# Performance work log

Measured on AMD Instinct MI355X. Metric: run time of the kernel, lower is better.

Reference implementation:

```python
import jax, jax.numpy as jnp
import numpy as np

B, S, DIM = 1, 4096, 4096
H, HL, D = 32, 8, 128          # query heads, kv heads (GQA), head_dim
BS = 8                          # sparse_block_size
SINK_TOK, WIN_TOK = 30, 30
HEAVY = 800                     # heavy_const -> Mb = HEAVY // BS top blocks
NEG = -1e30


def setup_inputs() -> dict:
    key = jax.random.key(0)
    k0, k1, k2, k3 = jax.random.split(key, 4)
    x = jax.random.normal(k0, (B, S, DIM), jnp.float32)
    freqs_cis = jax.random.uniform(k1, (S, D // 2, 2), jnp.float32)  # (cos,sin)-like pairs
    wqkv_w = jax.random.normal(k2, ((H + 2 * HL) * D, DIM), jnp.float32) * 0.02
    wo_w = jax.random.normal(k3, (DIM, DIM), jnp.float32) * 0.02
    input_pos = jnp.arange(S, dtype=jnp.int32)
    return {"x": x, "freqs_cis": freqs_cis, "wqkv_w": wqkv_w, "wo_w": wo_w, "input_pos": input_pos}


def _rope(x, fc):
    # x: [B,S,h,D], fc: [S,D/2,2]
    xr = x.reshape(*x.shape[:-1], -1, 2)            # [B,S,h,D/2,2]
    fc = fc[None, :, None]                           # [1,S,1,D/2,2]
    out = jnp.stack([xr[..., 0] * fc[..., 0] - xr[..., 1] * fc[..., 1],
                     xr[..., 1] * fc[..., 0] + xr[..., 0] * fc[..., 1]], axis=-1)
    return out.reshape(x.shape)


def reference(x, freqs_cis, wqkv_w, wo_w, input_pos):
    rep = H // HL
    Tb = (S + BS - 1) // BS
    scale = 1.0 / jnp.sqrt(jnp.float32(D))

    qkv = x @ wqkv_w.T                               # [B,S,(H+2HL)*D]
    q, k, v = jnp.split(qkv, [H * D, (H + HL) * D], axis=-1)
    q = q.reshape(B, S, H, D)
    k = k.reshape(B, S, HL, D)
    v = v.reshape(B, S, HL, D)
    q = _rope(q, freqs_cis)
    k = _rope(k, freqs_cis)

    # ---- block accumulators (KVCache.update_tokens), vectorized ----
    blk = input_pos // BS                            # [S]
    k_sum = jax.ops.segment_sum(jnp.swapaxes(k, 0, 1), blk, num_segments=Tb)  # [Tb,B,HL,D]
    cnt = jax.ops.segment_sum(jnp.ones((S,), jnp.float32), blk, num_segments=Tb)  # [Tb]
    k_rep = k_sum / jnp.maximum(cnt, 1.0)[:, None, None, None]                # block-mean keys
    k_rep_h = jnp.repeat(k_rep, rep, axis=2)        # [Tb,B,H,D] (GQA repeat)

    # ---- per-(B,H) block routing scores ----
    q_mean = q.mean(axis=1)                          # [B,H,D]
    scores = jnp.einsum('bhd,tbhd->bht', q_mean, k_rep_h) * scale  # [B,H,Tb]
    scores = jnp.where(cnt[None, None, :] > 0, scores, NEG)

    # ---- build_block_index: sink + window + topk ----
    sink_b = min((min(SINK_TOK, S) + BS - 1) // BS, Tb)
    window_b = min((min(WIN_TOK, S) + BS - 1) // BS, Tb)
    cur_block = (S - 1) // BS
    win_start = max(0, cur_block - window_b + 1)
    win_end = cur_block + 1
    sink_ids = jnp.arange(sink_b, dtype=jnp.int32)
    window_ids = jnp.arange(win_start, win_end, dtype=jnp.int32)
    Mb = max(0, min(HEAVY // BS, Tb))
    sc = scores.at[..., :sink_b].set(NEG).at[..., window_ids].set(NEG)
    top_ids = jax.lax.top_k(sc, Mb)[1].astype(jnp.int32)                      # [B,H,Mb]
    bidx = jnp.concatenate([
        jnp.broadcast_to(sink_ids, (B, H, sink_b)),
        jnp.broadcast_to(window_ids, (B, H, win_end - win_start)),
        top_ids], axis=-1)                           # [B,H,KLIST]

    # ---- gather selected block tokens ----
    tok = bidx[..., None] * BS + jnp.arange(BS, dtype=jnp.int32)              # [B,H,KLIST,BS]
    KL = bidx.shape[-1]
    tok = tok.reshape(B, H, KL * BS)                 # [B,H,Kt]
    valid = (tok >= 0) & (tok < S)
    tok_c = jnp.clip(tok, 0, S - 1)

    k_bhsd = jnp.swapaxes(jnp.repeat(k, rep, axis=2), 1, 2)  # [B,H,S,D]
    v_bhsd = jnp.swapaxes(jnp.repeat(v, rep, axis=2), 1, 2)
    Ksel = jnp.take_along_axis(k_bhsd, tok_c[..., None], axis=2)  # [B,H,Kt,D]
    Vsel = jnp.take_along_axis(v_bhsd, tok_c[..., None], axis=2)

    # ---- block-sparse attention with causal mask ----
    q_bhsd = jnp.swapaxes(q, 1, 2)                   # [B,H,S,D]
    att = jnp.einsum('bhsd,bhkd->bhsk', q_bhsd, Ksel) * scale
    mask = (tok_c[:, :, None, :] <= input_pos[None, None, :, None]) & valid[:, :, None, :]
    att = jnp.where(mask, att, NEG)
    p = jax.nn.softmax(att, axis=-1)
    out = jnp.einsum('bhsk,bhkd->bhsd', p, Vsel)     # [B,H,S,D]
    y = jnp.swapaxes(out, 1, 2).reshape(B, S, H * D) @ wo_w.T
    return y
```

## Files before the change

### kernel.cpp

```cpp
#include <hip/hip_runtime.h>
#include <hip/hip_bf16.h>

typedef unsigned short u16;
typedef unsigned int   u32;

using bf16x8 = __attribute__((ext_vector_type(8))) short;
using f32x4  = __attribute__((ext_vector_type(4))) float;

constexpr int S = 4096, DIM = 4096, H = 32, HL = 8, D = 128;
constexpr int NQKV = (H + 2 * HL) * D;
constexpr int QVW = (H + HL) * D;
constexpr int TB = S / 8;
constexpr int KL = 108;
constexpr float NEGF = -1e30f;
constexpr float SCALE = 0.08838834764831845f;

__device__ inline float bflo(u32 u) { return __builtin_bit_cast(float, u << 16); }
__device__ inline float bfhi(u32 u) { return __builtin_bit_cast(float, u & 0xFFFF0000u); }
__device__ inline u16 rne16(float f) {
  u32 b = __builtin_bit_cast(u32, f);
  return (u16)((b + 0x7FFFu + ((b >> 16) & 1u)) >> 16);
}
__device__ inline float bf2f(u16 h) { return __builtin_bit_cast(float, (u32)h << 16); }
__device__ inline u32 pk2(u16 a, u16 b) { return (u32)a | ((u32)b << 16); }

__device__ __forceinline__ void gload16(const u16* g, u16* l) {
  __builtin_amdgcn_global_load_lds(
      (__attribute__((address_space(1))) void*)g,
      (__attribute__((address_space(3))) void*)l, 16, 0, 0);
}

__device__ inline void xcd_swz(int nx, int& bx, int& by) {
  const int flat = blockIdx.y * nx + blockIdx.x;
  const int nwg = nx * gridDim.y;
  const int cpx = nwg >> 3;
  const int s = (flat & 7) * cpx + (flat >> 3);
  bx = s % nx;
  by = s / nx;
}

__global__ __launch_bounds__(256) void split_f32_kernel(
    const float* __restrict__ src, u16* __restrict__ hi, u16* __restrict__ lo) {
  const size_t i = ((size_t)blockIdx.x * 256 + threadIdx.x) * 8;
  float4 v0 = *(const float4*)(src + i);
  float4 v1 = *(const float4*)(src + i + 4);
  float f[8] = {v0.x, v0.y, v0.z, v0.w, v1.x, v1.y, v1.z, v1.w};
  u16 h[8], l[8];
#pragma unroll
  for (int j = 0; j < 8; ++j) {
    h[j] = rne16(f[j]);
    l[j] = rne16(f[j] - bf2f(h[j]));
  }
  uint4 ph, pl;
  ph.x = pk2(h[0], h[1]); ph.y = pk2(h[2], h[3]);
  ph.z = pk2(h[4], h[5]); ph.w = pk2(h[6], h[7]);
  pl.x = pk2(l[0], l[1]); pl.y = pk2(l[2], l[3]);
  pl.z = pk2(l[4], l[5]); pl.w = pk2(l[6], l[7]);
  *(uint4*)(hi + i) = ph;
  *(uint4*)(lo + i) = pl;
}

__global__ __launch_bounds__(256) void conv_wqkv_kernel(
    const float* __restrict__ src, u16* __restrict__ wqv,
    u16* __restrict__ wkh, u16* __restrict__ wkl) {
  const size_t i = ((size_t)blockIdx.x * 256 + threadIdx.x) * 8;
  float4 v0 = *(const float4*)(src + i);
  float4 v1 = *(const float4*)(src + i + 4);
  float f[8] = {v0.x, v0.y, v0.z, v0.w, v1.x, v1.y, v1.z, v1.w};
  u16 h[8];
#pragma unroll
  for (int j = 0; j < 8; ++j) h[j] = rne16(f[j]);
  uint4 ph;
  ph.x = pk2(h[0], h[1]); ph.y = pk2(h[2], h[3]);
  ph.z = pk2(h[4], h[5]); ph.w = pk2(h[6], h[7]);
  const int row = (int)(i >> 12);
  if (row < H * D) {
    *(uint4*)(wqv + i) = ph;
  } else if (row < (H + HL) * D) {
    const size_t off = i - (size_t)(H * D) * DIM;
    u16 l[8];
#pragma unroll
    for (int j = 0; j < 8; ++j) l[j] = rne16(f[j] - bf2f(h[j]));
    uint4 pl;
    pl.x = pk2(l[0], l[1]); pl.y = pk2(l[2], l[3]);
    pl.z = pk2(l[4], l[5]); pl.w = pk2(l[6], l[7]);
    *(uint4*)(wkh + off) = ph;
    *(uint4*)(wkl + off) = pl;
  } else {
    *(uint4*)(wqv + (i - (size_t)(HL * D) * DIM)) = ph;
  }
}

__global__ __launch_bounds__(256) void cast_bf16_kernel(
    const float* __restrict__ src, u16* __restrict__ dst) {
  const size_t i = ((size_t)blockIdx.x * 256 + threadIdx.x) * 8;
  float4 v0 = *(const float4*)(src + i);
  float4 v1 = *(const float4*)(src + i + 4);
  uint4 ph;
  ph.x = pk2(rne16(v0.x), rne16(v0.y));
  ph.y = pk2(rne16(v0.z), rne16(v0.w));
  ph.z = pk2(rne16(v1.x), rne16(v1.y));
  ph.w = pk2(rne16(v1.z), rne16(v1.w));
  *(uint4*)(dst + i) = ph;
}

template <bool OBF16>
__global__ __launch_bounds__(512, 2) void gemm256(
    const u16* __restrict__ A, const u16* __restrict__ B,
    void* __restrict__ Cp, int M, int N, int K, int lda, int ldb, int ldc) {
  __shared__ u16 lds[4 * 16384];
  const int tid = threadIdx.x;
  const int w = tid >> 6, lane = tid & 63;
  const int wm = w >> 2, wn = w & 3;
  const int l15 = lane & 15, g = lane >> 4;
  int bx, by;
  xcd_swz(gridDim.x, bx, by);
  const int m0 = by * 256, n0 = bx * 256;

  const u16* ga[4];
  const u16* gb[4];
#pragma unroll
  for (int r = 0; r < 4; ++r) {
    const int c = r * 512 + tid;
    const int row = c >> 3, j = c & 7;
    const int jsw = j ^ (row & 7);
    ga[r] = A + (size_t)(m0 + row) * lda + jsw * 8;
    gb[r] = B + (size_t)(n0 + row) * ldb + jsw * 8;
  }

  auto stageA = [&](int buf, int kt) {
    u16* base = lds + buf * 32768 + w * 512;
#pragma unroll
    for (int r = 0; r < 4; ++r) gload16(ga[r] + kt * 64, base + r * 4096);
  };
  auto stageB = [&](int buf, int kt) {
    u16* base = lds + buf * 32768 + 16384 + w * 512;
#pragma unroll
    for (int r = 0; r < 4; ++r) gload16(gb[r] + kt * 64, base + r * 4096);
  };

  bf16x8 afr[4][2], bfr[2][2];
  auto loadA = [&](int buf, int q) {
    const u16* Ab = lds + buf * 32768;
#pragma unroll
    for (int fr = 0; fr < 4; ++fr) {
      const int row = wm * 128 + q * 64 + fr * 16 + l15;
#pragma unroll
      for (int kh = 0; kh < 2; ++kh)
        afr[fr][kh] = *(const bf16x8*)(Ab + row * 64 + ((((kh << 2) | g)) ^ (l15 & 7)) * 8);
    }
  };
  auto loadB = [&](int buf, int r2) {
    const u16* Bb = lds + buf * 32768 + 16384;
#pragma unroll
    for (int fc = 0; fc < 2; ++fc) {
      const int row = wn * 64 + r2 * 32 + fc * 16 + l15;
#pragma unroll
      for (int kh = 0; kh < 2; ++kh)
        bfr[fc][kh] = *(const bf16x8*)(Bb + row * 64 + ((((kh << 2) | g)) ^ (l15 & 7)) * 8);
    }
  };

  f32x4 acc[8][4];
#pragma unroll
  for (int i = 0; i < 8; ++i)
#pragma unroll
    for (int j = 0; j < 4; ++j) acc[i][j] = {0.f, 0.f, 0.f, 0.f};

  auto mma = [&](int q, int r2) {
    __builtin_amdgcn_s_setprio(1);
#pragma unroll
    for (int fr = 0; fr < 4; ++fr)
#pragma unroll
      for (int fc = 0; fc < 2; ++fc)
#pragma unroll
        for (int kh = 0; kh < 2; ++kh)
          acc[q * 4 + fr][r2 * 2 + fc] = __builtin_amdgcn_mfma_f32_16x16x32_bf16(
              afr[fr][kh], bfr[fc][kh], acc[q * 4 + fr][r2 * 2 + fc], 0, 0, 0);
    __builtin_amdgcn_s_setprio(0);
  };

  stageA(0, 0);
  stageB(0, 0);
  const int NT = K / 64;
  for (int t = 0; t < NT; ++t) {
    const int cur = t & 1, nxt = cur ^ 1;
    if (t + 1 < NT) {
      stageA(nxt, t + 1);
      asm volatile("s_waitcnt vmcnt(4)" ::: "memory");
    } else {
      asm volatile("s_waitcnt vmcnt(0)" ::: "memory");
    }
    __builtin_amdgcn_sched_barrier(0);
    __builtin_amdgcn_s_barrier();
    loadA(cur, 0);
    loadB(cur, 0);
    mma(0, 0);
    __builtin_amdgcn_s_barrier();
    loadA(cur, 1);
    if (t + 1 < NT) stageB(nxt, t + 1);
    __builtin_amdgcn_s_barrier();
    mma(1, 0);
    __builtin_amdgcn_s_barrier();
    loadA(cur, 0);
    loadB(cur, 1);
    __builtin_amdgcn_s_barrier();
    mma(0, 1);
    __builtin_amdgcn_s_barrier();
    loadA(cur, 1);
    __builtin_amdgcn_s_barrier();
    mma(1, 1);
    __builtin_amdgcn_s_barrier();
  }
#pragma unroll
  for (int mf = 0; mf < 8; ++mf)
#pragma unroll
    for (int nf = 0; nf < 4; ++nf)
#pragma unroll
      for (int rg = 0; rg < 4; ++rg) {
        const int row = m0 + wm * 128 + mf * 16 + g * 4 + rg;
        const int col = n0 + wn * 64 + nf * 16 + l15;
        if constexpr (OBF16)
          ((u16*)Cp)[(size_t)row * ldc + col] = rne16(acc[mf][nf][rg]);
        else
          ((float*)Cp)[(size_t)row * ldc + col] = acc[mf][nf][rg];
      }
}

template <bool OBF16>
__global__ __launch_bounds__(256) void gemm_bf16(
    const u16* __restrict__ A, const u16* __restrict__ B,
    void* __restrict__ Cp, int M, int N, int K, int lda, int ldb, int ldc) {
  __shared__ u16 As[2][128 * 32];
  __shared__ u16 Bs[2][128 * 32];
  const int tid = threadIdx.x;
  const int lane = tid & 63;
  const int w = tid >> 6;
  const int wm = w >> 1, wn = w & 1;
  int bx, by;
  xcd_swz(gridDim.x, bx, by);
  const int m0 = by * 128, n0 = bx * 128;
  const int l15 = lane & 15, g = lane >> 4;
  const int srow = tid >> 2;
  const int scol = (tid & 3) * 8;

  const u16* ga = A + (size_t)(m0 + srow) * lda + scol;
  const u16* gb = B + (size_t)(n0 + srow) * ldb + scol;
  const size_t a64 = (size_t)64 * lda;
  const size_t b64 = (size_t)64 * ldb;

  auto stage = [&](int buf, int k0) {
    u16* lA = As[buf] + w * 512;
    u16* lB = Bs[buf] + w * 512;
    gload16(ga + k0, lA);
    gload16(ga + k0 + a64, lA + 2048);
    gload16(gb + k0, lB);
    gload16(gb + k0 + b64, lB + 2048);
  };

  f32x4 acc[4][4];
#pragma unroll
  for (int i = 0; i < 4; ++i)
#pragma unroll
    for (int j = 0; j < 4; ++j) acc[i][j] = {0.f, 0.f, 0.f, 0.f};

  stage(0, 0);
  __syncthreads();
  const int niter = K / 32;
  for (int it = 0; it < niter; ++it) {
    const int cur = it & 1;
    if (it + 1 < niter) stage(cur ^ 1, (it + 1) * 32);
    bf16x8 af[4], bfr[4];
#pragma unroll
    for (int i = 0; i < 4; ++i)
      af[i] = *(const bf16x8*)(As[cur] + (wm * 64 + i * 16 + l15) * 32 + g * 8);
#pragma unroll
    for (int j = 0; j < 4; ++j)
      bfr[j] = *(const bf16x8*)(Bs[cur] + (wn * 64 + j * 16 + l15) * 32 + g * 8);
#pragma unroll
    for (int i = 0; i < 4; ++i)
#pragma unroll
      for (int j = 0; j < 4; ++j)
        acc[i][j] = __builtin_amdgcn_mfma_f32_16x16x32_bf16(af[i], bfr[j], acc[i][j], 0, 0, 0);
    __syncthreads();
  }
#pragma unroll
  for (int i = 0; i < 4; ++i)
#pragma unroll
    for (int j = 0; j < 4; ++j)
#pragma unroll
      for (int rg = 0; rg < 4; ++rg) {
        const int row = m0 + wm * 64 + i * 16 + g * 4 + rg;
        const int col = n0 + wn * 64 + j * 16 + l15;
        if constexpr (OBF16)
          ((u16*)Cp)[(size_t)row * ldc + col] = rne16(acc[i][j][rg]);
        else
          ((float*)Cp)[(size_t)row * ldc + col] = acc[i][j][rg];
      }
}

__global__ __launch_bounds__(256) void gemm_k3(
    const u16* __restrict__ Ahg, const u16* __restrict__ Alg,
    const u16* __restrict__ Bhg, const u16* __restrict__ Blg,
    float* __restrict__ C, int M, int N, int K) {
  __shared__ u16 Ah[2][128 * 32];
  __shared__ u16 Al[2][128 * 32];
  __shared__ u16 Bh[2][64 * 32];
  __shared__ u16 Bl[2][64 * 32];
  const int tid = threadIdx.x;
  const int lane = tid & 63;
  const int w = tid >> 6;
  const int wm = w >> 1, wn = w & 1;
  int bx, by;
  xcd_swz(gridDim.x, bx, by);
  const int m0 = by * 128, n0 = bx * 64;
  const int l15 = lane & 15, g = lane >> 4;
  const int srow = tid >> 2;
  const int scol = (tid & 3) * 8;

  const u16* gah = Ahg + (size_t)(m0 + srow) * K + scol;
  const u16* gal = Alg + (size_t)(m0 + srow) * K + scol;
  const u16* gbh = Bhg + (size_t)(n0 + srow) * K + scol;
  const u16* gbl = Blg + (size_t)(n0 + srow) * K + scol;
  const size_t a64 = (size_t)64 * K;

  auto stage = [&](int buf, int k0) {
    gload16(gah + k0, Ah[buf] + w * 512);
    gload16(gah + k0 + a64, Ah[buf] + w * 512 + 2048);
    gload16(gal + k0, Al[buf] + w * 512);
    gload16(gal + k0 + a64, Al[buf] + w * 512 + 2048);
    gload16(gbh + k0, Bh[buf] + w * 512);
    gload16(gbl + k0, Bl[buf] + w * 512);
  };

  f32x4 acc[4][2];
#pragma unroll
  for (int i = 0; i < 4; ++i)
#pragma unroll
    for (int j = 0; j < 2; ++j) acc[i][j] = {0.f, 0.f, 0.f, 0.f};

  stage(0, 0);
  __syncthreads();
  const int niter = K / 32;
  for (int it = 0; it < niter; ++it) {
    const int cur = it & 1;
    if (it + 1 < niter) stage(cur ^ 1, (it + 1) * 32);
    bf16x8 fah[4], fal[4], fbh[2], fbl[2];
#pragma unroll
    for (int i = 0; i < 4; ++i) {
      fah[i] = *(const bf16x8*)(Ah[cur] + (wm * 64 + i * 16 + l15) * 32 + g * 8);
      fal[i] = *(const bf16x8*)(Al[cur] + (wm * 64 + i * 16 + l15) * 32 + g * 8);
    }
#pragma unroll
    for (int j = 0; j < 2; ++j) {
      fbh[j] = *(const bf16x8*)(Bh[cur] + (wn * 32 + j * 16 + l15) * 32 + g * 8);
      fbl[j] = *(const bf16x8*)(Bl[cur] + (wn * 32 + j * 16 + l15) * 32 + g * 8);
    }
#pragma unroll
    for (int i = 0; i < 4; ++i)
#pragma unroll
      for (int j = 0; j < 2; ++j) {
        acc[i][j] = __builtin_amdgcn_mfma_f32_16x16x32_bf16(fal[i], fbh[j], acc[i][j], 0, 0, 0);
        acc[i][j] = __builtin_amdgcn_mfma_f32_16x16x32_bf16(fah[i], fbl[j], acc[i][j], 0, 0, 0);
        acc[i][j] = __builtin_amdgcn_mfma_f32_16x16x32_bf16(fah[i], fbh[j], acc[i][j], 0, 0, 0);
      }
    __syncthreads();
  }
#pragma unroll
  for (int i = 0; i < 4; ++i)
#pragma unroll
    for (int j = 0; j < 2; ++j)
#pragma unroll
      for (int rg = 0; rg < 4; ++rg) {
        const int row = m0 + wm * 64 + i * 16 + g * 4 + rg;
        const int col = n0 + wn * 32 + j * 16 + l15;
        C[(size_t)row * N + col] = acc[i][j][rg];
      }
}

__global__ __launch_bounds__(128) void xcd_kernel(
    const float* __restrict__ x, const float* __restrict__ freqs,
    float* __restrict__ XC, float* __restrict__ XD) {
  const int d = blockIdx.x * 128 + threadIdx.x;
  const int i0 = blockIdx.y * 32;
  const int s0 = blockIdx.z * 128;
  float accC[32], accD[32];
#pragma unroll
  for (int ii = 0; ii < 32; ++ii) { accC[ii] = 0.f; accD[ii] = 0.f; }
  for (int s = s0; s < s0 + 128; ++s) {
    const float xv = x[(size_t)s * DIM + d];
    const float* fr = freqs + (size_t)s * 128 + i0 * 2;
#pragma unroll
    for (int ii = 0; ii < 32; ++ii) {
      accC[ii] += fr[2 * ii] * xv;
      accD[ii] += fr[2 * ii + 1] * xv;
    }
  }
#pragma unroll
  for (int ii = 0; ii < 32; ++ii) {
    atomicAdd(&XC[(size_t)(i0 + ii) * DIM + d], accC[ii]);
    atomicAdd(&XD[(size_t)(i0 + ii) * DIM + d], accD[ii]);
  }
}

__global__ __launch_bounds__(256) void mrow_kernel(
    const float* __restrict__ wq, const float* __restrict__ XC,
    const float* __restrict__ XD, float* __restrict__ M1, float* __restrict__ M2) {
  const int r = blockIdx.x * 4 + (threadIdx.x >> 6);
  const int lane = threadIdx.x & 63;
  const int i = (r & 127) >> 1;
  const float* wr = wq + (size_t)r * DIM;
  const float* xc = XC + (size_t)i * DIM;
  const float* xd = XD + (size_t)i * DIM;
  float s1 = 0.f, s2 = 0.f;
  for (int k = lane; k < DIM; k += 64) {
    float wv = wr[k];
    s1 += wv * xc[k];
    s2 += wv * xd[k];
  }
#pragma unroll
  for (int off = 1; off < 64; off <<= 1) {
    s1 += __shfl_xor(s1, off, 64);
    s2 += __shfl_xor(s2, off, 64);
  }
  if (lane == 0) { M1[r] = s1; M2[r] = s2; }
}

__global__ __launch_bounds__(256) void rope_q_kernel(
    const u16* __restrict__ qvb, const float* __restrict__ freqs,
    u16* __restrict__ qb) {
  const int h = blockIdx.y;
  const int s0 = blockIdx.x * 64;
  const int tid = threadIdx.x;
  const int d = tid & 127, half = tid >> 7;
  for (int pp = half; pp < 64; pp += 2) {
    const int s = s0 + pp;
    u32 pr = *(const u32*)(qvb + (size_t)s * QVW + h * D + (d & ~1));
    float a = bflo(pr), b = bfhi(pr);
    float2 fc = *(const float2*)(freqs + (size_t)s * 128 + (d & ~1));
    float o = (d & 1) ? (b * fc.x + a * fc.y) : (a * fc.x - b * fc.y);
    qb[((size_t)h * S + s) * D + d] = rne16(o);
  }
}

__global__ __launch_bounds__(128) void rope_kv_kernel(
    const float* __restrict__ kf, const u16* __restrict__ qvb,
    const float* __restrict__ freqs,
    u16* __restrict__ kb, u16* __restrict__ vbt, float* __restrict__ krep) {
  const int hl = blockIdx.y;
  const int t = blockIdx.x;
  const int d = threadIdx.x;
  float sum = 0.f;
  u16 vv[8];
#pragma unroll
  for (int pp = 0; pp < 8; ++pp) {
    const int s = t * 8 + pp;
    float2 kp = *(const float2*)(kf + (size_t)s * 1024 + hl * D + (d & ~1));
    float2 fc = *(const float2*)(freqs + (size_t)s * 128 + (d & ~1));
    float o = (d & 1) ? (kp.y * fc.x + kp.x * fc.y) : (kp.x * fc.x - kp.y * fc.y);
    kb[((size_t)hl * S + s) * D + d] = rne16(o);
    sum += o;
    vv[pp] = qvb[(size_t)s * QVW + H * D + hl * D + d];
  }
  krep[((size_t)t * HL + hl) * D + d] = sum * 0.125f;
  uint4 pk;
  pk.x = pk2(vv[0], vv[1]);
  pk.y = pk2(vv[2], vv[3]);
  pk.z = pk2(vv[4], vv[5]);
  pk.w = pk2(vv[6], vv[7]);
  *(uint4*)(vbt + ((size_t)hl * D + d) * S + t * 8) = pk;
}

__global__ __launch_bounds__(512) void topk_kernel(
    const float* __restrict__ M1, const float* __restrict__ M2,
    const float* __restrict__ krep, int* __restrict__ bidx) {
  const int h = blockIdx.x;
  const int t = threadIdx.x;
  __shared__ float qm[128];
  if (t < 128) {
    int r = h * 128 + t;
    float v = (t & 1) ? (M1[r] + M2[r - 1]) : (M1[r] - M2[r + 1]);
    qm[t] = v * (1.f / 4096.f);
  }
  __syncthreads();
  const float* kr = krep + ((size_t)t * HL + (h >> 2)) * 128;
  float s = 0.f;
#pragma unroll 8
  for (int d = 0; d < 128; ++d) s += qm[d] * kr[d];
  s *= SCALE;
  if (t < 4 || t >= 508) s = NEGF;
  if (t < 4) {
    bidx[h * KL + t] = t;
    bidx[h * KL + 4 + t] = 508 + t;
  }
  __shared__ float wv[8];
  __shared__ int wi[8];
  __shared__ int bestsh;
  for (int iter = 0; iter < 100; ++iter) {
    float v = s;
    int idx = t;
#pragma unroll
    for (int off = 1; off < 64; off <<= 1) {
      float ov = __shfl_xor(v, off, 64);
      int oi = __shfl_xor(idx, off, 64);
      if (ov > v || (ov == v && oi < idx)) { v = ov; idx = oi; }
    }
    if ((t & 63) == 0) { wv[t >> 6] = v; wi[t >> 6] = idx; }
    __syncthreads();
    if (t == 0) {
      float bv = wv[0];
      int bi = wi[0];
#pragma unroll
      for (int u = 1; u < 8; ++u)
        if (wv[u] > bv || (wv[u] == bv && wi[u] < bi)) { bv = wv[u]; bi = wi[u]; }
      bestsh = bi;
      bidx[h * KL + 8 + iter] = bi;
    }
    __syncthreads();
    if (t == bestsh) s = NEGF;
  }
}

__global__ __launch_bounds__(256) void attn_mfma(
    const u16* __restrict__ qb, const u16* __restrict__ kb,
    const u16* __restrict__ vbt, const int* __restrict__ bidx,
    u16* __restrict__ attno) {
  __shared__ u16 Ks[32][136];
  __shared__ u16 Vt[128][40];
  __shared__ u16 Ps[4][16][40];
  const int h = blockIdx.y, hl = h >> 2;
  const int q0 = blockIdx.x * 64;
  const int tid = threadIdx.x;
  const int w = tid >> 6, lane = tid & 63;
  const int l15 = lane & 15, g = lane >> 4;

  bf16x8 qf[4];
  {
    const u16* qp = qb + ((size_t)h * S + q0 + w * 16 + l15) * D + g * 8;
#pragma unroll
    for (int c = 0; c < 4; ++c) qf[c] = *(const bf16x8*)(qp + c * 32);
  }
  f32x4 o[8];
#pragma unroll
  for (int c = 0; c < 8; ++c) o[c] = {0.f, 0.f, 0.f, 0.f};
  float mrow[4], lrow[4];
#pragma unroll
  for (int r = 0; r < 4; ++r) { mrow[r] = NEGF; lrow[r] = 0.f; }

  for (int step = 0; step < KL / 4; ++step) {
    const int b0 = bidx[h * KL + step * 4 + 0];
    const int b1 = bidx[h * KL + step * 4 + 1];
    const int b2 = bidx[h * KL + step * 4 + 2];
    const int b3 = bidx[h * KL + step * 4 + 3];
    {
      const int tok = tid >> 3, seg = tid & 7;
      const int blk = (tok < 8) ? b0 : (tok < 16) ? b1 : (tok < 24) ? b2 : b3;
      const u16* src = kb + ((size_t)hl * S + blk * 8 + (tok & 7)) * D + seg * 16;
      *(uint4*)&Ks[tok][seg * 16] = *(const uint4*)src;
      *(uint4*)&Ks[tok][seg * 16 + 8] = *(const uint4*)(src + 8);
    }
    {
      const int d = tid >> 1, hf = tid & 1;
      const int ba = hf ? b2 : b0, bb = hf ? b3 : b1;
      const u16* src = vbt + ((size_t)hl * D + d) * S;
      *(uint4*)&Vt[d][hf * 16] = *(const uint4*)(src + ba * 8);
      *(uint4*)&Vt[d][hf * 16 + 8] = *(const uint4*)(src + bb * 8);
    }
    __syncthreads();
    f32x4 sA = {0.f, 0.f, 0.f, 0.f}, sB = {0.f, 0.f, 0.f, 0.f};
#pragma unroll
    for (int c = 0; c < 4; ++c) {
      bf16x8 k0 = *(const bf16x8*)&Ks[l15][c * 32 + g * 8];
      bf16x8 k1 = *(const bf16x8*)&Ks[16 + l15][c * 32 + g * 8];
      sA = __builtin_amdgcn_mfma_f32_16x16x32_bf16(qf[c], k0, sA, 0, 0, 0);
      sB = __builtin_amdgcn_mfma_f32_16x16x32_bf16(qf[c], k1, sB, 0, 0, 0);
    }
    const int tgA = ((l15 < 8) ? b0 : b1) * 8 + (l15 & 7);
    const int tgB = ((l15 < 8) ? b2 : b3) * 8 + (l15 & 7);
    float pA[4], pB[4], alpha[4];
#pragma unroll
    for (int r = 0; r < 4; ++r) {
      const int sq = q0 + w * 16 + g * 4 + r;
      pA[r] = (tgA <= sq) ? sA[r] * SCALE : NEGF;
      pB[r] = (tgB <= sq) ? sB[r] * SCALE : NEGF;
      float mx = fmaxf(pA[r], pB[r]);
      mx = fmaxf(mx, __shfl_xor(mx, 1, 64));
      mx = fmaxf(mx, __shfl_xor(mx, 2, 64));
      mx = fmaxf(mx, __shfl_xor(mx, 4, 64));
      mx = fmaxf(mx, __shfl_xor(mx, 8, 64));
      const float mnew = fmaxf(mrow[r], mx);
      alpha[r] = __expf(mrow[r] - mnew);
      mrow[r] = mnew;
      pA[r] = __expf(pA[r] - mnew);
      pB[r] = __expf(pB[r] - mnew);
      float rs = pA[r] + pB[r];
      rs += __shfl_xor(rs, 1, 64);
      rs += __shfl_xor(rs, 2, 64);
      rs += __shfl_xor(rs, 4, 64);
      rs += __shfl_xor(rs, 8, 64);
      lrow[r] = lrow[r] * alpha[r] + rs;
    }
#pragma unroll
    for (int c = 0; c < 8; ++c) {
      o[c][0] *= alpha[0]; o[c][1] *= alpha[1];
      o[c][2] *= alpha[2]; o[c][3] *= alpha[3];
    }
#pragma unroll
    for (int r = 0; r < 4; ++r) {
      Ps[w][g * 4 + r][l15] = rne16(pA[r]);
      Ps[w][g * 4 + r][16 + l15] = rne16(pB[r]);
    }
    bf16x8 pf = *(const bf16x8*)&Ps[w][l15][g * 8];
#pragma unroll
    for (int c = 0; c < 8; ++c) {
      bf16x8 vf = *(const bf16x8*)&Vt[c * 16 + l15][g * 8];
      o[c] = __builtin_amdgcn_mfma_f32_16x16x32_bf16(pf, vf, o[c], 0, 0, 0);
    }
    __syncthreads();
  }
  float inv[4];
#pragma unroll
  for (int r = 0; r < 4; ++r) inv[r] = 1.f / lrow[r];
#pragma unroll
  for (int c = 0; c < 8; ++c)
#pragma unroll
    for (int r = 0; r < 4; ++r)
      attno[(size_t)(q0 + w * 16 + g * 4 + r) * DIM + h * D + c * 16 + l15] =
          rne16(o[c][r] * inv[r]);
}

extern "C" void kernel_launch(void* const* d_in, const int* in_sizes, int n_in,
                              void* d_out, int out_size, void* d_ws, size_t ws_size,
                              hipStream_t stream) {
  const float* x     = (const float*)d_in[0];
  const float* freqs = (const float*)d_in[1];
  const float* wqkv  = (const float*)d_in[2];
  const float* wo    = (const float*)d_in[3];
  float* out = (float*)d_out;

  char* p = (char*)d_ws;
  auto alloc = [&](size_t bytes) {
    char* r = p;
    p += (bytes + 255) & ~(size_t)255;
    return r;
  };
  u16*   xh   = (u16*)alloc((size_t)S * DIM * 2);
  u16*   xl   = (u16*)alloc((size_t)S * DIM * 2);
  u16*   wqv  = (u16*)alloc((size_t)QVW * DIM * 2);
  u16*   wkh  = (u16*)alloc((size_t)HL * D * DIM * 2);
  u16*   wkl  = (u16*)alloc((size_t)HL * D * DIM * 2);
  u16*   wob  = (u16*)alloc((size_t)DIM * DIM * 2);
  u16*   qvb  = (u16*)alloc((size_t)S * QVW * 2);
  float* kf32 = (float*)alloc((size_t)S * HL * D * 4);
  u16*   qb   = (u16*)alloc((size_t)H * S * D * 2);
  u16*   kb   = (u16*)alloc((size_t)HL * S * D * 2);
  u16*   vbt  = (u16*)alloc((size_t)HL * D * S * 2);
  float* krep = (float*)alloc((size_t)TB * HL * D * 4);
  float* XC   = (float*)alloc((size_t)64 * DIM * 4);
  float* XD   = (float*)alloc((size_t)64 * DIM * 4);
  float* M1   = (float*)alloc((size_t)H * D * 4);
  float* M2   = (float*)alloc((size_t)H * D * 4);
  int*   bidx = (int*)alloc((size_t)H * KL * 4);
  u16*   attno = (u16*)alloc((size_t)S * DIM * 2);

  hipMemsetAsync(XC, 0, (size_t)64 * DIM * 4, stream);
  hipMemsetAsync(XD, 0, (size_t)64 * DIM * 4, stream);

  split_f32_kernel<<<(S * DIM) / 2048, 256, 0, stream>>>(x, xh, xl);
  conv_wqkv_kernel<<<(NQKV * DIM) / 2048, 256, 0, stream>>>(wqkv, wqv, wkh, wkl);
  cast_bf16_kernel<<<(DIM * DIM) / 2048, 256, 0, stream>>>(wo, wob);

  gemm256<true><<<dim3((H * D) / 256, S / 256), 512, 0, stream>>>(
      xh, wqv, qvb, S, H * D, DIM, DIM, DIM, QVW);
  gemm_bf16<true><<<dim3((HL * D) / 128, S / 128), 256, 0, stream>>>(
      xh, wqv + (size_t)(H * D) * DIM, qvb + H * D, S, HL * D, DIM, DIM, DIM, QVW);

  gemm_k3<<<dim3((HL * D) / 64, S / 128), 256, 0, stream>>>(
      xh, xl, wkh, wkl, kf32, S, HL * D, DIM);

  xcd_kernel<<<dim3(32, 2, 32), 128, 0, stream>>>(x, freqs, XC, XD);
  mrow_kernel<<<1024, 256, 0, stream>>>(wqkv, XC, XD, M1, M2);
  rope_q_kernel<<<dim3(S / 64, H), 256, 0, stream>>>(qvb, freqs, qb);
  rope_kv_kernel<<<dim3(TB, HL), 128, 0, stream>>>(kf32, qvb, freqs, kb, vbt, krep);
  topk_kernel<<<H, 512, 0, stream>>>(M1, M2, krep, bidx);
  attn_mfma<<<dim3(S / 64, H), 256, 0, stream>>>(qb, kb, vbt, bidx, attno);
  gemm256<false><<<dim3(DIM / 256, S / 256), 512, 0, stream>>>(
      attno, wob, out, S, DIM, DIM, DIM, DIM, DIM);
}
```

Baseline: 1.267 ms.

## Double-buffer K/V via registers, widen attention tile to 64 tokens, lazy rescale

The sparse attention kernel now processes eight selected blocks per iteration instead of four. It prefetches the next tile's K and V into registers while computing the current tile, then stores them to shared memory after the barrier. The online softmax skips rescaling the output accumulators unless some row's max grows by more than a threshold. This is meant to hide gather latency and cut per-step barriers and exp work, at the cost of more registers and shared memory, which may reduce occupancy.

```diff
diff --git a/kernel.cpp b/kernel.cpp
--- a/kernel.cpp
+++ b/kernel.cpp
@@ -525,14 +525,15 @@
     const u16* __restrict__ qb, const u16* __restrict__ kb,
     const u16* __restrict__ vbt, const int* __restrict__ bidx,
     u16* __restrict__ attno) {
-  __shared__ u16 Ks[32][136];
-  __shared__ u16 Vt[128][40];
-  __shared__ u16 Ps[4][16][40];
+  __shared__ u16 Ks[64][136];
+  __shared__ u16 Vt[128][72];
+  __shared__ u16 Ps[4][16][72];
   const int h = blockIdx.y, hl = h >> 2;
   const int q0 = blockIdx.x * 64;
   const int tid = threadIdx.x;
   const int w = tid >> 6, lane = tid & 63;
   const int l15 = lane & 15, g = lane >> 4;
+  constexpr int NS = (KL + 7) / 8;
 
   bf16x8 qf[4];
   {
@@ -547,76 +548,126 @@
 #pragma unroll
   for (int r = 0; r < 4; ++r) { mrow[r] = NEGF; lrow[r] = 0.f; }
 
-  for (int step = 0; step < KL / 4; ++step) {
-    const int b0 = bidx[h * KL + step * 4 + 0];
-    const int b1 = bidx[h * KL + step * 4 + 1];
-    const int b2 = bidx[h * KL + step * 4 + 2];
-    const int b3 = bidx[h * KL + step * 4 + 3];
-    {
-      const int tok = tid >> 3, seg = tid & 7;
-      const int blk = (tok < 8) ? b0 : (tok < 16) ? b1 : (tok < 24) ? b2 : b3;
-      const u16* src = kb + ((size_t)hl * S + blk * 8 + (tok & 7)) * D + seg * 16;
-      *(uint4*)&Ks[tok][seg * 16] = *(const uint4*)src;
-      *(uint4*)&Ks[tok][seg * 16 + 8] = *(const uint4*)(src + 8);
-    }
-    {
-      const int d = tid >> 1, hf = tid & 1;
-      const int ba = hf ? b2 : b0, bb = hf ? b3 : b1;
-      const u16* src = vbt + ((size_t)hl * D + d) * S;
-      *(uint4*)&Vt[d][hf * 16] = *(const uint4*)(src + ba * 8);
-      *(uint4*)&Vt[d][hf * 16 + 8] = *(const uint4*)(src + bb * 8);
-    }
-    __syncthreads();
-    f32x4 sA = {0.f, 0.f, 0.f, 0.f}, sB = {0.f, 0.f, 0.f, 0.f};
-#pragma unroll
-    for (int c = 0; c < 4; ++c) {
-      bf16x8 k0 = *(const bf16x8*)&Ks[l15][c * 32 + g * 8];
-      bf16x8 k1 = *(const bf16x8*)&Ks[16 + l15][c * 32 + g * 8];
-      sA = __builtin_amdgcn_mfma_f32_16x16x32_bf16(qf[c], k0, sA, 0, 0, 0);
-      sB = __builtin_amdgcn_mfma_f32_16x16x32_bf16(qf[c], k1, sB, 0, 0, 0);
-    }
-    const int tgA = ((l15 < 8) ? b0 : b1) * 8 + (l15 & 7);
-    const int tgB = ((l15 < 8) ? b2 : b3) * 8 + (l15 & 7);
-    float pA[4], pB[4], alpha[4];
+  const int ktok = tid >> 2, kq = tid & 3;
+  const int vd = tid >> 1, vh = tid & 1;
+
+  int tb[8];
+  int tbn[8];
+  uint4 kreg[4], vreg[4];
+
+  auto issue = [&](int t8) {
+#pragma unroll
+    for (int s = 0; s < 8; ++s) {
+      const int st = t8 + s;
+      tbn[s] = (st < KL) ? bidx[h * KL + st] * 8 : S + 8;
+    }
+    const int kslot = t8 + (ktok >> 3);
+    const int kblk = (kslot < KL) ? bidx[h * KL + kslot] : 0;
+    const u16* ksrc = kb + ((size_t)hl * S + kblk * 8 + (ktok & 7)) * D + kq * 32;
+#pragma unroll
+    for (int j = 0; j < 4; ++j) kreg[j] = *(const uint4*)(ksrc + j * 8);
+    const u16* vsrc = vbt + ((size_t)hl * D + vd) * S;
+#pragma unroll
+    for (int j = 0; j < 4; ++j) {
+      const int vslot = t8 + vh * 4 + j;
+      const int vblk = (vslot < KL) ? bidx[h * KL + vslot] : 0;
+      vreg[j] = *(const uint4*)(vsrc + (size_t)vblk * 8);
+    }
+  };
+  auto store = [&]() {
+#pragma unroll
+    for (int j = 0; j < 4; ++j) *(uint4*)&Ks[ktok][kq * 32 + j * 8] = kreg[j];
+#pragma unroll
+    for (int j = 0; j < 4; ++j) *(uint4*)&Vt[vd][vh * 32 + j * 8] = vreg[j];
+  };
+
+  issue(0);
+  store();
+#pragma unroll
+  for (int s = 0; s < 8; ++s) tb[s] = tbn[s];
+  __syncthreads();
+
+  for (int t = 0; t < NS; ++t) {
+    const bool hasNext = (t + 1 < NS);
+    if (hasNext) issue((t + 1) * 8);
+
+    f32x4 sT[4];
+#pragma unroll
+    for (int ti = 0; ti < 4; ++ti) sT[ti] = {0.f, 0.f, 0.f, 0.f};
+#pragma unroll
+    for (int c = 0; c < 4; ++c)
+#pragma unroll
+      for (int ti = 0; ti < 4; ++ti) {
+        bf16x8 kf = *(const bf16x8*)&Ks[ti * 16 + l15][c * 32 + g * 8];
+        sT[ti] = __builtin_amdgcn_mfma_f32_16x16x32_bf16(qf[c], kf, sT[ti], 0, 0, 0);
+      }
+
+    int tg[4];
+#pragma unroll
+    for (int ti = 0; ti < 4; ++ti)
+      tg[ti] = ((l15 & 8) ? tb[ti * 2 + 1] : tb[ti * 2]) + (l15 & 7);
+    float p[4][4], mx[4];
 #pragma unroll
     for (int r = 0; r < 4; ++r) {
       const int sq = q0 + w * 16 + g * 4 + r;
-      pA[r] = (tgA <= sq) ? sA[r] * SCALE : NEGF;
-      pB[r] = (tgB <= sq) ? sB[r] * SCALE : NEGF;
-      float mx = fmaxf(pA[r], pB[r]);
-      mx = fmaxf(mx, __shfl_xor(mx, 1, 64));
-      mx = fmaxf(mx, __shfl_xor(mx, 2, 64));
-      mx = fmaxf(mx, __shfl_xor(mx, 4, 64));
-      mx = fmaxf(mx, __shfl_xor(mx, 8, 64));
-      const float mnew = fmaxf(mrow[r], mx);
-      alpha[r] = __expf(mrow[r] - mnew);
-      mrow[r] = mnew;
-      pA[r] = __expf(pA[r] - mnew);
-      pB[r] = __expf(pB[r] - mnew);
-      float rs = pA[r] + pB[r];
+      float m = NEGF;
+#pragma unroll
+      for (int ti = 0; ti < 4; ++ti) {
+        p[r][ti] = (tg[ti] <= sq) ? sT[ti][r] * SCALE : NEGF;
+        m = fmaxf(m, p[r][ti]);
+      }
+      m = fmaxf(m, __shfl_xor(m, 1, 64));
+      m = fmaxf(m, __shfl_xor(m, 2, 64));
+      m = fmaxf(m, __shfl_xor(m, 4, 64));
+      m = fmaxf(m, __shfl_xor(m, 8, 64));
+      mx[r] = m;
+    }
+    const bool need = (mx[0] > mrow[0] + 8.f) | (mx[1] > mrow[1] + 8.f) |
+                      (mx[2] > mrow[2] + 8.f) | (mx[3] > mrow[3] + 8.f);
+    if (__any((int)need)) {
+#pragma unroll
+      for (int r = 0; r < 4; ++r) {
+        const float mnew = fmaxf(mrow[r], mx[r]);
+        const float alpha = __expf(mrow[r] - mnew);
+        mrow[r] = mnew;
+        lrow[r] *= alpha;
+#pragma unroll
+        for (int c = 0; c < 8; ++c) o[c][r] *= alpha;
+      }
+    }
+#pragma unroll
+    for (int r = 0; r < 4; ++r) {
+      float rs = 0.f;
+#pragma unroll
+      for (int ti = 0; ti < 4; ++ti) {
+        p[r][ti] = __expf(p[r][ti] - mrow[r]);
+        rs += p[r][ti];
+      }
       rs += __shfl_xor(rs, 1, 64);
       rs += __shfl_xor(rs, 2, 64);
       rs += __shfl_xor(rs, 4, 64);
       rs += __shfl_xor(rs, 8, 64);
-      lrow[r] = lrow[r] * alpha[r] + rs;
-    }
+      lrow[r] += rs;
+#pragma unroll
+      for (int ti = 0; ti < 4; ++ti)
+        Ps[w][g * 4 + r][ti * 16 + l15] = rne16(p[r][ti]);
+    }
+    bf16x8 pf0 = *(const bf16x8*)&Ps[w][l15][g * 8];
+    bf16x8 pf1 = *(const bf16x8*)&Ps[w][l15][32 + g * 8];
 #pragma unroll
     for (int c = 0; c < 8; ++c) {
-      o[c][0] *= alpha[0]; o[c][1] *= alpha[1];
-      o[c][2] *= alpha[2]; o[c][3] *= alpha[3];
-    }
-#pragma unroll
-    for (int r = 0; r < 4; ++r) {
-      Ps[w][g * 4 + r][l15] = rne16(pA[r]);
-      Ps[w][g * 4 + r][16 + l15] = rne16(pB[r]);
-    }
-    bf16x8 pf = *(const bf16x8*)&Ps[w][l15][g * 8];
-#pragma unroll
-    for (int c = 0; c < 8; ++c) {
-      bf16x8 vf = *(const bf16x8*)&Vt[c * 16 + l15][g * 8];
-      o[c] = __builtin_amdgcn_mfma_f32_16x16x32_bf16(pf, vf, o[c], 0, 0, 0);
+      bf16x8 v0 = *(const bf16x8*)&Vt[c * 16 + l15][g * 8];
+      bf16x8 v1 = *(const bf16x8*)&Vt[c * 16 + l15][32 + g * 8];
+      o[c] = __builtin_amdgcn_mfma_f32_16x16x32_bf16(pf0, v0, o[c], 0, 0, 0);
+      o[c] = __builtin_amdgcn_mfma_f32_16x16x32_bf16(pf1, v1, o[c], 0, 0, 0);
     }
     __syncthreads();
+    if (hasNext) {
+      store();
+#pragma unroll
+      for (int s = 0; s < 8; ++s) tb[s] = tbn[s];
+      __syncthreads();
+    }
   }
   float inv[4];
 #pragma unroll
```

Result: slower. 1.461 ms (+15.2%).
